# Kernel optimization log

Measured on AMD Instinct MI355X. Metric: run time of the kernel, lower is better.

The kernel has to match this reference:

```python
import jax, jax.numpy as jnp
import numpy as np
from functools import partial

B, T_DEC, S_ENC = 64, 30, 31
E, U, V = 128, 256, 32000

def setup_inputs() -> dict:
    key = jax.random.key(0)
    ks = jax.random.split(key, 12)
    sc = lambda *s: 1.0 / np.sqrt(s[0])
    return {
        "inputs": jax.random.randint(ks[0], (B, T_DEC), 0, V, dtype=jnp.int64),
        "memory": jax.random.normal(ks[1], (B, S_ENC, U), jnp.float32),
        "sample_h": jax.random.normal(ks[2], (B, U), jnp.float32),
        "sample_c": jax.random.normal(ks[3], (B, U), jnp.float32),
        "emb_table": jax.random.normal(ks[4], (V, E), jnp.float32) * 0.02,
        "W_k": jax.random.normal(ks[5], (E + U, 4 * U), jnp.float32) * sc(E + U),
        "W_r": jax.random.normal(ks[6], (U, 4 * U), jnp.float32) * sc(U),
        "b_lstm": jnp.zeros((4 * U,), jnp.float32),
        "W_mem": jax.random.normal(ks[7], (U, U), jnp.float32) * sc(U),
        "W_attn": jax.random.normal(ks[8], (2 * U, U), jnp.float32) * sc(2 * U),
        "W_fc": jax.random.normal(ks[9], (U, V), jnp.float32) * sc(U),
        "b_fc": jnp.zeros((V,), jnp.float32),
    }

def _decode(inputs, memory, sample_h, sample_c, emb_table, W_k, W_r, b_lstm,
            W_mem, W_attn, W_fc, b_fc):
    # Luong attention keys: memory_layer(memory), no bias. [B,S,U]
    keys = jnp.einsum('bsu,uv->bsv', memory, W_mem)
    x_emb = emb_table[inputs]                       # [B,T,E]
    xs = jnp.swapaxes(x_emb, 0, 1)                  # [T,B,E]

    def step(carry, x_t):
        h, c, attn = carry
        # AttentionWrapper cell_input_fn: concat(input, prev_attention)
        cell_in = jnp.concatenate([x_t, attn], axis=-1)           # [B,E+U]
        z = cell_in @ W_k + h @ W_r + b_lstm                      # [B,4U]
        i, f, g, o = jnp.split(z, 4, axis=-1)
        c = jax.nn.sigmoid(f) * c + jax.nn.sigmoid(i) * jnp.tanh(g)
        h = jax.nn.sigmoid(o) * jnp.tanh(c)
        # Luong score: query . keys ; memory_sequence_length covers all S, no mask
        score = jnp.einsum('bu,bsu->bs', h, keys)                 # [B,S]
        align = jax.nn.softmax(score, axis=-1)
        context = jnp.einsum('bs,bsu->bu', align, memory)         # [B,U]
        # attention_layer: Dense(U, use_bias=False) on concat(cell_out, context)
        attn = jnp.concatenate([h, context], axis=-1) @ W_attn    # [B,U]
        out_t = attn @ W_fc + b_fc                                # [B,V]
        return (h, c, attn), out_t

    init = (sample_h, sample_c, jnp.zeros((sample_h.shape[0], U), sample_h.dtype))
    _, outs = jax.lax.scan(step, init, xs)          # [T,B,V]
    return jnp.swapaxes(outs, 0, 1)                 # [B,T,V]

def reference(inputs, memory, sample_h, sample_c, emb_table, W_k, W_r, b_lstm,
              W_mem, W_attn, W_fc, b_fc):
    return _decode(inputs, memory, sample_h, sample_c, emb_table, W_k, W_r,
                   b_lstm, W_mem, W_attn, W_fc, b_fc)
```

## Files before the change

### kernel.cpp

```cpp
#include <hip/hip_runtime.h>
#include <hip/hip_bf16.h>
#include <math.h>

constexpr int NB = 64;
constexpr int NT = 30;
constexpr int NS = 31;
constexpr int NE = 128;
constexpr int NU = 256;
constexpr int NV = 32000;
constexpr int NG = 4 * NU;

typedef unsigned short u16;
typedef __attribute__((ext_vector_type(8))) short bf16x8;
typedef __attribute__((ext_vector_type(4))) float f32x4;

__device__ __forceinline__ float sigmoidf_(float x) {
    return 1.0f / (1.0f + __expf(-x));
}

__device__ __forceinline__ u16 rne_bf16(float x) {
    unsigned u = __float_as_uint(x);
    unsigned r = u + 0x7fffu + ((u >> 16) & 1u);
    return (u16)(r >> 16);
}

__global__ __launch_bounds__(256) void keys_kernel(
    const float* __restrict__ memory, const float* __restrict__ W_mem,
    float* __restrict__ keys) {
    const int row0 = blockIdx.x * 8;
    const int u = threadIdx.x;
    __shared__ float mS[8][NU];
#pragma unroll
    for (int r = 0; r < 8; ++r) mS[r][u] = memory[(row0 + r) * NU + u];
    __syncthreads();
    float acc[8] = {0, 0, 0, 0, 0, 0, 0, 0};
#pragma unroll 4
    for (int v = 0; v < NU; ++v) {
        float w = W_mem[v * NU + u];
#pragma unroll
        for (int r = 0; r < 8; ++r) acc[r] += mS[r][v] * w;
    }
#pragma unroll
    for (int r = 0; r < 8; ++r) keys[(row0 + r) * NU + u] = acc[r];
}

__global__ __launch_bounds__(256) void fuse_wz_kernel(
    const float* __restrict__ W_k,
    const float* __restrict__ W_r,
    const float* __restrict__ W_a,
    float* __restrict__ Wzp)
{
    const int col = blockIdx.x * 256 + threadIdx.x;
    const int rb = blockIdx.y * 8;
    __shared__ float waS[8][NU];
#pragma unroll
    for (int r = 0; r < 8; ++r) waS[r][threadIdx.x] = W_a[(size_t)(rb + r) * NU + threadIdx.x];
    __syncthreads();
    float acc[8] = {};
#pragma unroll 4
    for (int j = 0; j < NU; ++j) {
        float w = W_k[(size_t)(NE + j) * NG + col];
#pragma unroll
        for (int r = 0; r < 8; ++r) acc[r] += waS[r][j] * w;
    }
    const int gate = col >> 8, u = col & 255;
    const int qb = u >> 6, lc = gate * 64 + (u & 63);
#pragma unroll
    for (int r = 0; r < 8; ++r) {
        int i = rb + r;
        float v = acc[r];
        if (i < NU) v += W_r[(size_t)i * NG + col];
        Wzp[(size_t)qb * 512 * 256 + (size_t)i * 256 + lc] = v;
    }
}

__global__ __launch_bounds__(256) void zemb_kernel(
    const int* __restrict__ inputs, const float* __restrict__ emb,
    const float* __restrict__ W_k, const float* __restrict__ b_lstm,
    float* __restrict__ z_emb)
{
    const int col = blockIdx.x * 256 + threadIdx.x;
    const int m0 = blockIdx.y * 8;
    __shared__ float eS[8][NE];
    for (int i = threadIdx.x; i < 8 * NE; i += 256) {
        int r = i >> 7, e = i & 127;
        eS[r][e] = emb[(size_t)inputs[m0 + r] * NE + e];
    }
    __syncthreads();
    float acc[8] = {};
#pragma unroll 4
    for (int e = 0; e < NE; ++e) {
        float w = W_k[(size_t)e * NG + col];
#pragma unroll
        for (int r = 0; r < 8; ++r) acc[r] += eS[r][e] * w;
    }
    float bb = b_lstm[col];
#pragma unroll
    for (int r = 0; r < 8; ++r) z_emb[(size_t)(m0 + r) * NG + col] = acc[r] + bb;
}

__global__ __launch_bounds__(1024, 4) void recurrence_coop(
    const float* __restrict__ z_emb,
    const float* __restrict__ sample_h,
    const float* __restrict__ sample_c,
    const float* __restrict__ Wzp,
    const float* __restrict__ W_r,
    const float* __restrict__ memory,
    const float* __restrict__ keys,
    float* __restrict__ h_all,
    float* __restrict__ ctx_all,
    unsigned* __restrict__ bar)
{
    const int bid = blockIdx.x;
    const int b  = bid & 63;
    const int qb = bid >> 6;
    const int tid = threadIdx.x;

    __shared__ float memS[NS * NU];
    __shared__ float zPart[16 * 256];
    __shared__ float actS[2 * NU];
    __shared__ float scS[32];

    const float* memb = memory + (size_t)b * NS * NU;
    const float* keyb = keys + (size_t)b * NS * NU;
    for (int i = tid; i < NS * NU / 4; i += 1024)
        ((float4*)memS)[i] = ((const float4*)memb)[i];
    if (tid < NU) actS[tid] = sample_h[b * NU + tid];
    float c_reg = (tid < 64) ? sample_c[b * NU + qb * 64 + tid] : 0.0f;

    const int colq = tid & 63;
    const int p    = tid >> 6;
    const int gate = colq >> 4, wq = colq & 15;
    const int ncol = gate * 256 + qb * 64 + wq * 4;
    const float* panel = Wzp + (size_t)qb * 512 * 256;
    const float* zerow = z_emb + (size_t)(b * NT) * NG + ncol;
    unsigned* ctr = bar + b;

    __syncthreads();

    for (int t = 0; t < NT; ++t) {
        {
            float4 acc = (p == 0) ? *(const float4*)(zerow + (size_t)t * NG)
                                  : make_float4(0.f, 0.f, 0.f, 0.f);
            if (t == 0) {
                const float* ap = actS + p * 16;
#pragma unroll
                for (int k = 0; k < 16; ++k) {
                    float a = ap[k];
                    float4 w = *(const float4*)(W_r + (size_t)(p * 16 + k) * NG + ncol);
                    acc.x += a * w.x; acc.y += a * w.y;
                    acc.z += a * w.z; acc.w += a * w.w;
                }
            } else {
                const float* ap = actS + p * 32;
                const float* wp = panel + (size_t)(p * 32) * 256 + colq * 4;
#pragma unroll 8
                for (int k = 0; k < 32; ++k) {
                    float a = ap[k];
                    float4 w = *(const float4*)(wp + k * 256);
                    acc.x += a * w.x; acc.y += a * w.y;
                    acc.z += a * w.z; acc.w += a * w.w;
                }
            }
            *(float4*)(zPart + p * 256 + colq * 4) = acc;
        }
        __syncthreads();

        const size_t m = (size_t)b * NT + t;
        if (tid < 64) {
            float zv[4];
#pragma unroll
            for (int g = 0; g < 4; ++g) {
                float s = 0.f;
#pragma unroll
                for (int q = 0; q < 16; ++q) s += zPart[q * 256 + g * 64 + tid];
                zv[g] = s;
            }
            c_reg = sigmoidf_(zv[1]) * c_reg + sigmoidf_(zv[0]) * tanhf(zv[2]);
            float h = sigmoidf_(zv[3]) * tanhf(c_reg);
            __hip_atomic_store(h_all + m * NU + qb * 64 + tid, h,
                               __ATOMIC_RELAXED, __HIP_MEMORY_SCOPE_AGENT);
        }
        __syncthreads();

        if (tid == 0) {
            __hip_atomic_fetch_add(ctr, 1u, __ATOMIC_RELAXED,
                                   __HIP_MEMORY_SCOPE_AGENT);
            const unsigned tgt = 4u * (unsigned)(t + 1);
            while (__hip_atomic_load(ctr, __ATOMIC_RELAXED,
                                     __HIP_MEMORY_SCOPE_AGENT) < tgt)
                __builtin_amdgcn_s_sleep(2);
        }
        __syncthreads();

        if (tid < NU)
            actS[tid] = __hip_atomic_load(h_all + m * NU + tid,
                                          __ATOMIC_RELAXED,
                                          __HIP_MEMORY_SCOPE_AGENT);
        __syncthreads();

        {
            const int s = tid >> 5, j = tid & 31;
            if (s < NS) {
                float sp = 0.0f;
#pragma unroll
                for (int i = 0; i < 8; ++i)
                    sp += actS[i * 32 + j] * keyb[s * NU + i * 32 + j];
#pragma unroll
                for (int msk = 16; msk; msk >>= 1) sp += __shfl_xor(sp, msk, 32);
                if (j == 0) scS[s] = sp;
            }
        }
        __syncthreads();

        if (tid < NU) {
            float mx = scS[0];
#pragma unroll
            for (int s = 1; s < NS; ++s) mx = fmaxf(mx, scS[s]);
            float sumE = 0.0f, ctx = 0.0f;
#pragma unroll 4
            for (int s = 0; s < NS; ++s) {
                float e = __expf(scS[s] - mx);
                sumE += e;
                ctx += e * memS[s * NU + tid];
            }
            ctx /= sumE;
            actS[NU + tid] = ctx;
            if (qb == 0) ctx_all[m * NU + tid] = ctx;
        }
        __syncthreads();
    }
}

__global__ __launch_bounds__(256) void attn_kernel(
    const float* __restrict__ h_all, const float* __restrict__ ctx_all,
    const float* __restrict__ W_a, float* __restrict__ attn_all,
    u16* __restrict__ Ahl)
{
    const int j = threadIdx.x;
    const int m0 = blockIdx.x * 8;
    __shared__ float hS[8][NU], cS[8][NU];
    for (int i = j; i < 8 * NU; i += 256) {
        int r = i >> 8, k = i & 255;
        hS[r][k] = h_all[(size_t)(m0 + r) * NU + k];
        cS[r][k] = ctx_all[(size_t)(m0 + r) * NU + k];
    }
    __syncthreads();
    float acc[8] = {};
#pragma unroll 2
    for (int k = 0; k < NU; ++k) {
        float w1 = W_a[(size_t)k * NU + j];
        float w2 = W_a[(size_t)(NU + k) * NU + j];
#pragma unroll
        for (int r = 0; r < 8; ++r) acc[r] += hS[r][k] * w1 + cS[r][k] * w2;
    }
#pragma unroll
    for (int r = 0; r < 8; ++r) {
        float a = acc[r];
        size_t m = (size_t)(m0 + r) * NU + j;
        attn_all[m] = a;
        u16 h = rne_bf16(a);
        float hf = __uint_as_float((unsigned)h << 16);
        Ahl[m] = h;
        Ahl[(size_t)NB * NT * NU + m] = rne_bf16(a - hf);
    }
}

__global__ __launch_bounds__(256) void wfc_pack(
    const float* __restrict__ Wfc, u16* __restrict__ Bt)
{
    const int n0 = blockIdx.x * 64;
    const int tid = threadIdx.x;
    __shared__ __align__(16) u16 tS[64][264];

#pragma unroll
    for (int part = 0; part < 2; ++part) {
        for (int kk = 0; kk < 256; kk += 4) {
            int k = kk + (tid >> 6);
            int n = tid & 63;
            float v = Wfc[(size_t)k * NV + n0 + n];
            u16 h = rne_bf16(v);
            u16 w = h;
            if (part) {
                float hf = __uint_as_float((unsigned)h << 16);
                w = rne_bf16(v - hf);
            }
            tS[n][k] = w;
        }
        __syncthreads();
        {
            int n = tid >> 2;
#pragma unroll
            for (int i = 0; i < 8; ++i) {
                int c = (tid & 3) + i * 4;
                *(uint4*)(Bt + (size_t)(n0 + n) * 512 + part * 256 + c * 8) =
                    *(const uint4*)(&tS[n][c * 8]);
            }
        }
        __syncthreads();
    }
}

__global__ __launch_bounds__(256) void out_gemm_mfma(
    const u16* __restrict__ Ahl,
    const u16* __restrict__ Bt,
    const float* __restrict__ bfc,
    float* __restrict__ out)
{
    constexpr int NWG = (NV / 128) * ((NB * NT) / 128);
    constexpr int qq = NWG / 8, rr = NWG % 8;
    int bid = blockIdx.x;
    int xcd = bid & 7, idx = bid >> 3;
    int wg = (xcd < rr ? xcd * (qq + 1) : rr * (qq + 1) + (xcd - rr) * qq) + idx;
    const int nt = wg / 15, mt = wg % 15;
    const int n0 = nt * 128, m0 = mt * 128;

    const int tid = threadIdx.x;
    const int wave = tid >> 6, lane = tid & 63;
    const int wm = wave >> 1, wn = wave & 1;
    const int l15 = lane & 15, lq = lane >> 4;

    constexpr size_t ALOFF = (size_t)NB * NT * NU;

    const u16* arow[4];
    const u16* brow[4];
#pragma unroll
    for (int f = 0; f < 4; ++f) {
        arow[f] = Ahl + (size_t)(m0 + wm * 64 + f * 16 + l15) * 256 + lq * 8;
        brow[f] = Bt + (size_t)(n0 + wn * 64 + f * 16 + l15) * 512 + lq * 8;
    }

    f32x4 acc[4][4] = {};

#pragma unroll
    for (int kk = 0; kk < 8; ++kk) {
        bf16x8 ah[4], al[4], bh[4], bl[4];
#pragma unroll
        for (int f = 0; f < 4; ++f) {
            ah[f] = *(const bf16x8*)(arow[f] + kk * 32);
            al[f] = *(const bf16x8*)(arow[f] + ALOFF + kk * 32);
            bh[f] = *(const bf16x8*)(brow[f] + kk * 32);
            bl[f] = *(const bf16x8*)(brow[f] + 256 + kk * 32);
        }
#pragma unroll
        for (int i = 0; i < 4; ++i)
#pragma unroll
            for (int j = 0; j < 4; ++j) {
                acc[i][j] = __builtin_amdgcn_mfma_f32_16x16x32_bf16(
                    ah[i], bh[j], acc[i][j], 0, 0, 0);
                acc[i][j] = __builtin_amdgcn_mfma_f32_16x16x32_bf16(
                    al[i], bh[j], acc[i][j], 0, 0, 0);
                acc[i][j] = __builtin_amdgcn_mfma_f32_16x16x32_bf16(
                    ah[i], bl[j], acc[i][j], 0, 0, 0);
            }
    }

    float bias[4];
#pragma unroll
    for (int j = 0; j < 4; ++j) bias[j] = bfc[n0 + wn * 64 + j * 16 + l15];
#pragma unroll
    for (int i = 0; i < 4; ++i) {
        const int mrow = m0 + wm * 64 + i * 16 + lq * 4;
#pragma unroll
        for (int j = 0; j < 4; ++j) {
            const size_t base = (size_t)mrow * NV + n0 + wn * 64 + j * 16 + l15;
#pragma unroll
            for (int rg = 0; rg < 4; ++rg)
                out[base + (size_t)rg * NV] = acc[i][j][rg] + bias[j];
        }
    }
}

constexpr int BM = 128, BN = 128, KC = 32, KTOT = NU;

__global__ __launch_bounds__(256) void out_gemm(
    const float* __restrict__ A,
    const float* __restrict__ Wfc,
    const float* __restrict__ bfc,
    float* __restrict__ out)
{
    const int n0 = blockIdx.x * BN;
    const int m0 = blockIdx.y * BM;
    const int tid = threadIdx.x;
    const int tx = tid & 15, ty = tid >> 4;

    __shared__ float As[KC][BM + 4];
    __shared__ float Bs[KC][BN];

    float acc[2][4][2][4] = {};

    const int kq = tid & 7,  r0 = tid >> 3;
    const int nq = tid & 31, kr0 = tid >> 5;

    float4 aR[4], bR[4];

#pragma unroll
    for (int p = 0; p < 4; ++p)
        aR[p] = *(const float4*)(A + (size_t)(m0 + r0 + p * 32) * KTOT + kq * 4);
#pragma unroll
    for (int p = 0; p < 4; ++p)
        bR[p] = *(const float4*)(Wfc + (size_t)(kr0 + p * 8) * NV + n0 + nq * 4);
#pragma unroll
    for (int p = 0; p < 4; ++p) {
        int r = r0 + p * 32;
        As[kq * 4 + 0][r] = aR[p].x;
        As[kq * 4 + 1][r] = aR[p].y;
        As[kq * 4 + 2][r] = aR[p].z;
        As[kq * 4 + 3][r] = aR[p].w;
        *(float4*)&Bs[kr0 + p * 8][nq * 4] = bR[p];
    }
    __syncthreads();

    for (int kb = 0; kb < KTOT; kb += KC) {
        const bool more = (kb + KC) < KTOT;
        if (more) {
#pragma unroll
            for (int p = 0; p < 4; ++p)
                aR[p] = *(const float4*)(A + (size_t)(m0 + r0 + p * 32) * KTOT + kb + KC + kq * 4);
#pragma unroll
            for (int p = 0; p < 4; ++p)
                bR[p] = *(const float4*)(Wfc + (size_t)(kb + KC + kr0 + p * 8) * NV + n0 + nq * 4);
        }

#pragma unroll 4
        for (int k = 0; k < KC; ++k) {
            float4 a0 = *(const float4*)&As[k][ty * 4];
            float4 a1 = *(const float4*)&As[k][64 + ty * 4];
            float4 b0 = *(const float4*)&Bs[k][tx * 4];
            float4 b1 = *(const float4*)&Bs[k][64 + tx * 4];
            float am[2][4] = {{a0.x, a0.y, a0.z, a0.w}, {a1.x, a1.y, a1.z, a1.w}};
            float bv[2][4] = {{b0.x, b0.y, b0.z, b0.w}, {b1.x, b1.y, b1.z, b1.w}};
#pragma unroll
            for (int im = 0; im < 2; ++im)
#pragma unroll
                for (int i = 0; i < 4; ++i)
#pragma unroll
                    for (int jn = 0; jn < 2; ++jn)
#pragma unroll
                        for (int j = 0; j < 4; ++j)
                            acc[im][i][jn][j] += am[im][i] * bv[jn][j];
        }
        __syncthreads();

        if (more) {
#pragma unroll
            for (int p = 0; p < 4; ++p) {
                int r = r0 + p * 32;
                As[kq * 4 + 0][r] = aR[p].x;
                As[kq * 4 + 1][r] = aR[p].y;
                As[kq * 4 + 2][r] = aR[p].z;
                As[kq * 4 + 3][r] = aR[p].w;
                *(float4*)&Bs[kr0 + p * 8][nq * 4] = bR[p];
            }
            __syncthreads();
        }
    }

    float4 bias[2];
    bias[0] = *(const float4*)(bfc + n0 + tx * 4);
    bias[1] = *(const float4*)(bfc + n0 + 64 + tx * 4);
#pragma unroll
    for (int im = 0; im < 2; ++im)
#pragma unroll
        for (int i = 0; i < 4; ++i) {
            int m = m0 + im * 64 + ty * 4 + i;
#pragma unroll
            for (int jn = 0; jn < 2; ++jn) {
                float4 v;
                float4 bb = bias[jn];
                v.x = acc[im][i][jn][0] + bb.x;
                v.y = acc[im][i][jn][1] + bb.y;
                v.z = acc[im][i][jn][2] + bb.z;
                v.w = acc[im][i][jn][3] + bb.w;
                *(float4*)(out + (size_t)m * NV + n0 + jn * 64 + tx * 4) = v;
            }
        }
}

extern "C" void kernel_launch(void* const* d_in, const int* in_sizes, int n_in,
                              void* d_out, int out_size, void* d_ws, size_t ws_size,
                              hipStream_t stream) {
    const int*   inputs   = (const int*)  d_in[0];
    const float* memory   = (const float*)d_in[1];
    const float* sample_h = (const float*)d_in[2];
    const float* sample_c = (const float*)d_in[3];
    const float* emb      = (const float*)d_in[4];
    const float* W_k      = (const float*)d_in[5];
    const float* W_r      = (const float*)d_in[6];
    const float* b_lstm   = (const float*)d_in[7];
    const float* W_mem    = (const float*)d_in[8];
    const float* W_attn   = (const float*)d_in[9];
    const float* W_fc     = (const float*)d_in[10];
    const float* b_fc     = (const float*)d_in[11];
    float* out = (float*)d_out;

    constexpr size_t SZ_KEYS = (size_t)NB * NS * NU;
    constexpr size_t SZ_WZ   = (size_t)4 * 512 * 256;
    constexpr size_t SZ_ZEMB = (size_t)NB * NT * NG;
    constexpr size_t SZ_ACT  = (size_t)NB * NT * NU;
    constexpr size_t SZ_AHL  = SZ_ACT;
    constexpr size_t SZ_BAR  = 64;
    constexpr size_t SZ_BT   = (size_t)NV * 512 / 2;

    float* keys     = (float*)d_ws;
    float* Wzp      = keys + SZ_KEYS;
    float* z_emb    = Wzp + SZ_WZ;
    float* h_all    = z_emb + SZ_ZEMB;
    float* ctx_all  = h_all + SZ_ACT;
    float* attn_all = ctx_all + SZ_ACT;
    u16*   Ahl      = (u16*)(attn_all + SZ_ACT);
    unsigned* bar   = (unsigned*)(attn_all + SZ_ACT + SZ_AHL);
    float* bt_f     = attn_all + SZ_ACT + SZ_AHL + SZ_BAR;
    u16*   Bt       = (u16*)bt_f;

    const size_t need_bytes =
        (SZ_KEYS + SZ_WZ + SZ_ZEMB + 3 * SZ_ACT + SZ_AHL + SZ_BAR + SZ_BT) * 4;
    const bool use_mfma = ws_size >= need_bytes;

    keys_kernel<<<(NB * NS) / 8, 256, 0, stream>>>(memory, W_mem, keys);
    fuse_wz_kernel<<<dim3(NG / 256, (2 * NU) / 8), 256, 0, stream>>>(W_k, W_r,
                                                                     W_attn, Wzp);
    zemb_kernel<<<dim3(NG / 256, (NB * NT) / 8), 256, 0, stream>>>(inputs, emb,
                                                                   W_k, b_lstm,
                                                                   z_emb);
    if (use_mfma)
        wfc_pack<<<NV / 64, 256, 0, stream>>>(W_fc, Bt);

    hipMemsetAsync(bar, 0, NB * sizeof(unsigned), stream);

    {
        void* kargs[] = {
            (void*)&z_emb, (void*)&sample_h, (void*)&sample_c, (void*)&Wzp,
            (void*)&W_r, (void*)&memory, (void*)&keys, (void*)&h_all,
            (void*)&ctx_all, (void*)&bar
        };
        hipLaunchCooperativeKernel((const void*)recurrence_coop,
                                   dim3(NB * 4), dim3(1024), kargs, 0, stream);
    }

    attn_kernel<<<(NB * NT) / 8, 256, 0, stream>>>(h_all, ctx_all, W_attn,
                                                   attn_all, Ahl);

    if (use_mfma) {
        out_gemm_mfma<<<(NV / 128) * ((NB * NT) / 128), 256, 0, stream>>>(
            Ahl, Bt, b_fc, out);
    } else {
        out_gemm<<<dim3(NV / BN, (NB * NT) / BM), 256, 0, stream>>>(
            attn_all, W_fc, b_fc, out);
    }
}
```

Measured before the change: 940.4 us.

## Cache keys and weights on-chip in recurrence, coalesce GEMM epilogue stores

The recurrence kernel now copies each batch's attention keys into shared memory and keeps part of the recurrent weight panel in registers across timesteps, so each step issues fewer global loads. The gate-partial reduction is spread over 256 threads instead of 64. The output GEMM epilogue stages its accumulators through shared memory so rows are written as coalesced float4 stores with bias. The weight-packing kernel writes its high and low bf16 halves in one pass. In exchange the kernels use more shared memory and registers and add barriers, which may lower occupancy.

```diff
diff --git a/kernel.cpp b/kernel.cpp
--- a/kernel.cpp
+++ b/kernel.cpp
@@ -98,6 +98,8 @@
 #pragma unroll
     for (int r = 0; r < 8; ++r) z_emb[(size_t)(m0 + r) * NG + col] = acc[r] + bb;
 }
+
+constexpr int WS = 10;
 
 __global__ __launch_bounds__(1024, 4) void recurrence_coop(
     const float* __restrict__ z_emb,
@@ -117,14 +119,18 @@
     const int tid = threadIdx.x;
 
     __shared__ float memS[NS * NU];
+    __shared__ float keyS[NS * NU];
     __shared__ float zPart[16 * 256];
+    __shared__ float zS[256];
     __shared__ float actS[2 * NU];
     __shared__ float scS[32];
 
     const float* memb = memory + (size_t)b * NS * NU;
     const float* keyb = keys + (size_t)b * NS * NU;
-    for (int i = tid; i < NS * NU / 4; i += 1024)
+    for (int i = tid; i < NS * NU / 4; i += 1024) {
         ((float4*)memS)[i] = ((const float4*)memb)[i];
+        ((float4*)keyS)[i] = ((const float4*)keyb)[i];
+    }
     if (tid < NU) actS[tid] = sample_h[b * NU + tid];
     float c_reg = (tid < 64) ? sample_c[b * NU + qb * 64 + tid] : 0.0f;
 
@@ -133,51 +139,67 @@
     const int gate = colq >> 4, wq = colq & 15;
     const int ncol = gate * 256 + qb * 64 + wq * 4;
     const float* panel = Wzp + (size_t)qb * 512 * 256;
+    const float* wp = panel + (size_t)(p * 32) * 256 + colq * 4;
     const float* zerow = z_emb + (size_t)(b * NT) * NG + ncol;
     unsigned* ctr = bar + b;
 
+    float4 wreg[WS];
+#pragma unroll
+    for (int k = 0; k < WS; ++k) wreg[k] = *(const float4*)(wp + (size_t)k * 256);
+
     __syncthreads();
 
     for (int t = 0; t < NT; ++t) {
         {
-            float4 acc = (p == 0) ? *(const float4*)(zerow + (size_t)t * NG)
-                                  : make_float4(0.f, 0.f, 0.f, 0.f);
+            float4 accr = (p == 0) ? *(const float4*)(zerow + (size_t)t * NG)
+                                   : make_float4(0.f, 0.f, 0.f, 0.f);
             if (t == 0) {
                 const float* ap = actS + p * 16;
 #pragma unroll
                 for (int k = 0; k < 16; ++k) {
                     float a = ap[k];
                     float4 w = *(const float4*)(W_r + (size_t)(p * 16 + k) * NG + ncol);
-                    acc.x += a * w.x; acc.y += a * w.y;
-                    acc.z += a * w.z; acc.w += a * w.w;
+                    accr.x += a * w.x; accr.y += a * w.y;
+                    accr.z += a * w.z; accr.w += a * w.w;
                 }
+                *(float4*)(zPart + p * 256 + colq * 4) = accr;
             } else {
                 const float* ap = actS + p * 32;
-                const float* wp = panel + (size_t)(p * 32) * 256 + colq * 4;
-#pragma unroll 8
-                for (int k = 0; k < 32; ++k) {
+                float4 accs = make_float4(0.f, 0.f, 0.f, 0.f);
+#pragma unroll 11
+                for (int k = WS; k < 32; ++k) {
                     float a = ap[k];
-                    float4 w = *(const float4*)(wp + k * 256);
-                    acc.x += a * w.x; acc.y += a * w.y;
-                    acc.z += a * w.z; acc.w += a * w.w;
+                    float4 w = *(const float4*)(wp + (size_t)k * 256);
+                    accs.x += a * w.x; accs.y += a * w.y;
+                    accs.z += a * w.z; accs.w += a * w.w;
                 }
+#pragma unroll
+                for (int k = 0; k < WS; ++k) {
+                    float a = ap[k];
+                    accr.x += a * wreg[k].x; accr.y += a * wreg[k].y;
+                    accr.z += a * wreg[k].z; accr.w += a * wreg[k].w;
+                }
+                accr.x += accs.x; accr.y += accs.y;
+                accr.z += accs.z; accr.w += accs.w;
+                *(float4*)(zPart + p * 256 + colq * 4) = accr;
             }
-            *(float4*)(zPart + p * 256 + colq * 4) = acc;
+        }
+        __syncthreads();
+
+        if (tid < 256) {
+            float s = 0.f;
+#pragma unroll
+            for (int q = 0; q < 16; ++q) s += zPart[q * 256 + tid];
+            zS[tid] = s;
         }
         __syncthreads();
 
         const size_t m = (size_t)b * NT + t;
         if (tid < 64) {
-            float zv[4];
-#pragma unroll
-            for (int g = 0; g < 4; ++g) {
-                float s = 0.f;
-#pragma unroll
-                for (int q = 0; q < 16; ++q) s += zPart[q * 256 + g * 64 + tid];
-                zv[g] = s;
-            }
-            c_reg = sigmoidf_(zv[1]) * c_reg + sigmoidf_(zv[0]) * tanhf(zv[2]);
-            float h = sigmoidf_(zv[3]) * tanhf(c_reg);
+            float zi = zS[tid], zf = zS[64 + tid];
+            float zg = zS[128 + tid], zo = zS[192 + tid];
+            c_reg = sigmoidf_(zf) * c_reg + sigmoidf_(zi) * tanhf(zg);
+            float h = sigmoidf_(zo) * tanhf(c_reg);
             __hip_atomic_store(h_all + m * NU + qb * 64 + tid, h,
                                __ATOMIC_RELAXED, __HIP_MEMORY_SCOPE_AGENT);
         }
@@ -205,7 +227,7 @@
                 float sp = 0.0f;
 #pragma unroll
                 for (int i = 0; i < 8; ++i)
-                    sp += actS[i * 32 + j] * keyb[s * NU + i * 32 + j];
+                    sp += actS[i * 32 + j] * keyS[s * NU + i * 32 + j];
 #pragma unroll
                 for (int msk = 16; msk; msk >>= 1) sp += __shfl_xor(sp, msk, 32);
                 if (j == 0) scS[s] = sp;
@@ -271,33 +293,29 @@
 {
     const int n0 = blockIdx.x * 64;
     const int tid = threadIdx.x;
-    __shared__ __align__(16) u16 tS[64][264];
-
-#pragma unroll
-    for (int part = 0; part < 2; ++part) {
-        for (int kk = 0; kk < 256; kk += 4) {
-            int k = kk + (tid >> 6);
-            int n = tid & 63;
-            float v = Wfc[(size_t)k * NV + n0 + n];
-            u16 h = rne_bf16(v);
-            u16 w = h;
-            if (part) {
-                float hf = __uint_as_float((unsigned)h << 16);
-                w = rne_bf16(v - hf);
-            }
-            tS[n][k] = w;
-        }
-        __syncthreads();
-        {
-            int n = tid >> 2;
-#pragma unroll
-            for (int i = 0; i < 8; ++i) {
-                int c = (tid & 3) + i * 4;
-                *(uint4*)(Bt + (size_t)(n0 + n) * 512 + part * 256 + c * 8) =
-                    *(const uint4*)(&tS[n][c * 8]);
-            }
-        }
-        __syncthreads();
+    __shared__ __align__(16) u16 tSh[64][264];
+    __shared__ __align__(16) u16 tSl[64][264];
+
+    for (int kk = 0; kk < 256; kk += 4) {
+        int k = kk + (tid >> 6);
+        int n = tid & 63;
+        float v = Wfc[(size_t)k * NV + n0 + n];
+        u16 h = rne_bf16(v);
+        float hf = __uint_as_float((unsigned)h << 16);
+        tSh[n][k] = h;
+        tSl[n][k] = rne_bf16(v - hf);
+    }
+    __syncthreads();
+    {
+        int n = tid >> 2;
+#pragma unroll
+        for (int i = 0; i < 8; ++i) {
+            int c = (tid & 3) + i * 4;
+            *(uint4*)(Bt + (size_t)(n0 + n) * 512 + c * 8) =
+                *(const uint4*)(&tSh[n][c * 8]);
+            *(uint4*)(Bt + (size_t)(n0 + n) * 512 + 256 + c * 8) =
+                *(const uint4*)(&tSl[n][c * 8]);
+        }
     }
 }
 
@@ -355,19 +373,31 @@
             }
     }
 
-    float bias[4];
-#pragma unroll
-    for (int j = 0; j < 4; ++j) bias[j] = bfc[n0 + wn * 64 + j * 16 + l15];
-#pragma unroll
-    for (int i = 0; i < 4; ++i) {
-        const int mrow = m0 + wm * 64 + i * 16 + lq * 4;
-#pragma unroll
-        for (int j = 0; j < 4; ++j) {
-            const size_t base = (size_t)mrow * NV + n0 + wn * 64 + j * 16 + l15;
-#pragma unroll
-            for (int rg = 0; rg < 4; ++rg)
-                out[base + (size_t)rg * NV] = acc[i][j][rg] + bias[j];
-        }
+    __shared__ float cT[64][132];
+    const int cq = tid & 31, r8 = tid >> 5;
+    float4 bb = *(const float4*)(bfc + n0 + cq * 4);
+
+#pragma unroll
+    for (int hm = 0; hm < 2; ++hm) {
+        if (wm == hm) {
+#pragma unroll
+            for (int i = 0; i < 4; ++i)
+#pragma unroll
+                for (int j = 0; j < 4; ++j)
+#pragma unroll
+                    for (int rg = 0; rg < 4; ++rg)
+                        cT[i * 16 + lq * 4 + rg][wn * 64 + j * 16 + l15] =
+                            acc[i][j][rg];
+        }
+        __syncthreads();
+#pragma unroll
+        for (int it = 0; it < 8; ++it) {
+            int r = it * 8 + r8;
+            float4 v = *(const float4*)&cT[r][cq * 4];
+            v.x += bb.x; v.y += bb.y; v.z += bb.z; v.w += bb.w;
+            *(float4*)(out + (size_t)(m0 + hm * 64 + r) * NV + n0 + cq * 4) = v;
+        }
+        __syncthreads();
     }
 }
 
```

Measured after the change: 967.4 us. 2.9% more time.
